# Kernel optimization log

Measured on AMD Instinct MI355X. Metric: run time of the kernel, lower is better.

Reference implementation:

```python
import jax, jax.numpy as jnp
import numpy as np

# Static config matching Fp8Padding(num_gemms=8, align_size=16)
M_SPLITS = [4091, 8177, 2045, 4093, 6133, 1021, 4085, 8189]
ALIGN = 16
PADDED_M_SPLITS = [(m + ALIGN - 1) // ALIGN * ALIGN for m in M_SPLITS]
HIDDEN = 2048
TOTAL_IN = sum(M_SPLITS)      # 37834
TOTAL_OUT = sum(PADDED_M_SPLITS)  # 37888


def _build_gather_idx() -> np.ndarray:
    """For each padded output row: source row index in inp, or -1 for pad rows."""
    idx = np.full(TOTAL_OUT, -1, dtype=np.int32)
    src = 0
    dst = 0
    for m, p in zip(M_SPLITS, PADDED_M_SPLITS):
        idx[dst:dst + m] = np.arange(src, src + m, dtype=np.int32)
        src += m
        dst += p
    return idx

_IDX = _build_gather_idx()


def setup_inputs() -> dict:
    key = jax.random.key(0)
    inp = jax.random.normal(key, (TOTAL_IN, HIDDEN), dtype=jnp.float32)
    return {"inp": inp}


def reference(inp):
    # Single coalesced multi-segment copy: gather source rows into padded
    # offsets, zero-fill the alignment padding rows.
    idx = jnp.asarray(_IDX)                      # [TOTAL_OUT]
    valid = (idx >= 0)[:, None]                  # [TOTAL_OUT, 1]
    out = jnp.where(valid, inp[jnp.clip(idx, 0), :], jnp.zeros((), inp.dtype))
    return out  # [TOTAL_OUT, HIDDEN]; padded_m_splits is the static PADDED_M_SPLITS
```

## Files before the change

kernel.cpp:

```cpp
#include <hip/hip_runtime.h>


constexpr int HIDDEN   = 2048;
constexpr int HIDDEN4  = HIDDEN / 4;
constexpr int NSEG     = 8;
constexpr int TOTAL_OUT = 37888;

__device__ __constant__ int d_dst[NSEG + 1] =
    {0, 4096, 12288, 14336, 18432, 24576, 25600, 29696, 37888};
__device__ __constant__ int d_srcs[NSEG] =
    {0, 4091, 12268, 14313, 18406, 24539, 25560, 29645};
__device__ __constant__ int d_m[NSEG] =
    {4091, 8177, 2045, 4093, 6133, 1021, 4085, 8189};

__global__ __launch_bounds__(256) void fp8_pad_copy(
    const float* __restrict__ in, float* __restrict__ out) {
    const int row = blockIdx.x;

    int seg = 0;
#pragma unroll
    for (int s = 1; s < NSEG; ++s) seg += (row >= d_dst[s]) ? 1 : 0;

    const int local = row - d_dst[seg];
    const int srow  = (local < d_m[seg]) ? (d_srcs[seg] + local) : -1;

    const float4* __restrict__ in4  = reinterpret_cast<const float4*>(in);
    float4* __restrict__       out4 = reinterpret_cast<float4*>(out);
    const long ro = (long)row * HIDDEN4;

    if (srow >= 0) {
        const long si = (long)srow * HIDDEN4;
#pragma unroll
        for (int t = threadIdx.x; t < HIDDEN4; t += 256) {
            out4[ro + t] = in4[si + t];
        }
    } else {
        const float4 z = make_float4(0.f, 0.f, 0.f, 0.f);
#pragma unroll
        for (int t = threadIdx.x; t < HIDDEN4; t += 256) {
            out4[ro + t] = z;
        }
    }
}

extern "C" void kernel_launch(void* const* d_in, const int* in_sizes, int n_in,
                              void* d_out, int out_size, void* d_ws, size_t ws_size,
                              hipStream_t stream) {
    const float* in = reinterpret_cast<const float*>(d_in[0]);
    float* out      = reinterpret_cast<float*>(d_out);
    fp8_pad_copy<<<TOTAL_OUT, 256, 0, stream>>>(in, out);
}
```

Measured before the change: 484.1 us.

## Flatten padded copy into strided float4 stream with batched nontemporal loads

Replaces the one-block-per-row copy with a flat grid-stride scheme over float4 elements. Each thread resolves its segment with compile-time constants, issues eight nontemporal loads back to back, then eight nontemporal stores. This is meant to raise memory-level parallelism and keep cache pollution low on a purely bandwidth-bound copy. It relies on the hardcoded grid size covering the output exactly and adds per-element segment lookup arithmetic.

```diff
diff --git a/kernel.cpp b/kernel.cpp
--- a/kernel.cpp
+++ b/kernel.cpp
@@ -1,45 +1,50 @@
 #include <hip/hip_runtime.h>
 
 
-constexpr int HIDDEN   = 2048;
-constexpr int HIDDEN4  = HIDDEN / 4;
-constexpr int NSEG     = 8;
-constexpr int TOTAL_OUT = 37888;
+typedef float fvec4 __attribute__((ext_vector_type(4)));
 
-__device__ __constant__ int d_dst[NSEG + 1] =
-    {0, 4096, 12288, 14336, 18432, 24576, 25600, 29696, 37888};
-__device__ __constant__ int d_srcs[NSEG] =
-    {0, 4091, 12268, 14313, 18406, 24539, 25560, 29645};
-__device__ __constant__ int d_m[NSEG] =
-    {4091, 8177, 2045, 4093, 6133, 1021, 4085, 8189};
+constexpr int NSEG = 8;
+constexpr int DST4[NSEG + 1] = {0, 2097152, 6291456, 7340032, 9437184,
+                                12582912, 13107200, 15204352, 19398656};
+constexpr int SRC4[NSEG] = {0, 2094592, 6281216, 7328256,
+                            9423872, 12563968, 13086720, 15178240};
+constexpr int MLEN4[NSEG] = {2094592, 4186624, 1047040, 2095616,
+                             3140096, 522752, 2091520, 4192768};
 
-__global__ __launch_bounds__(256) void fp8_pad_copy(
-    const float* __restrict__ in, float* __restrict__ out) {
-    const int row = blockIdx.x;
+constexpr int BLOCKS = 9472;
+constexpr int TPB = 256;
+constexpr int K = 8;
+constexpr int STRIDE = BLOCKS * TPB;
 
-    int seg = 0;
+__global__ __launch_bounds__(TPB) void fp8_pad_copy(const float* __restrict__ in,
+                                                    float* __restrict__ out) {
+    const fvec4* __restrict__ in4 = reinterpret_cast<const fvec4*>(in);
+    fvec4* __restrict__ out4 = reinterpret_cast<fvec4*>(out);
+    const int tid = blockIdx.x * TPB + threadIdx.x;
+
+    fvec4 vals[K];
 #pragma unroll
-    for (int s = 1; s < NSEG; ++s) seg += (row >= d_dst[s]) ? 1 : 0;
-
-    const int local = row - d_dst[seg];
-    const int srow  = (local < d_m[seg]) ? (d_srcs[seg] + local) : -1;
-
-    const float4* __restrict__ in4  = reinterpret_cast<const float4*>(in);
-    float4* __restrict__       out4 = reinterpret_cast<float4*>(out);
-    const long ro = (long)row * HIDDEN4;
-
-    if (srow >= 0) {
-        const long si = (long)srow * HIDDEN4;
+    for (int k = 0; k < K; ++k) {
+        const int i = tid + k * STRIDE;
+        int dstb = DST4[0], srcb = SRC4[0], mlen = MLEN4[0];
 #pragma unroll
-        for (int t = threadIdx.x; t < HIDDEN4; t += 256) {
-            out4[ro + t] = in4[si + t];
+        for (int s = 1; s < NSEG; ++s) {
+            const bool ge = i >= DST4[s];
+            dstb = ge ? DST4[s] : dstb;
+            srcb = ge ? SRC4[s] : srcb;
+            mlen = ge ? MLEN4[s] : mlen;
         }
-    } else {
-        const float4 z = make_float4(0.f, 0.f, 0.f, 0.f);
+        const int local = i - dstb;
+        fvec4 v = {0.f, 0.f, 0.f, 0.f};
+        if (local < mlen) {
+            v = __builtin_nontemporal_load(&in4[srcb + local]);
+        }
+        vals[k] = v;
+    }
 #pragma unroll
-        for (int t = threadIdx.x; t < HIDDEN4; t += 256) {
-            out4[ro + t] = z;
-        }
+    for (int k = 0; k < K; ++k) {
+        const int i = tid + k * STRIDE;
+        __builtin_nontemporal_store(vals[k], &out4[i]);
     }
 }
 
@@ -47,6 +52,6 @@
                               void* d_out, int out_size, void* d_ws, size_t ws_size,
                               hipStream_t stream) {
     const float* in = reinterpret_cast<const float*>(d_in[0]);
-    float* out      = reinterpret_cast<float*>(d_out);
-    fp8_pad_copy<<<TOTAL_OUT, 256, 0, stream>>>(in, out);
+    float* out = reinterpret_cast<float*>(d_out);
+    fp8_pad_copy<<<BLOCKS, TPB, 0, stream>>>(in, out);
 }
```

Result: no change. 483.2 us (-0.2%).
